# Kernel optimization log

Hardware: AMD Instinct MI355X
Metric: run time of the kernel (lower is better)

The kernel has to match this reference:

```python
import jax, jax.numpy as jnp
import numpy as np
from jax import lax

RES = 7
SCALE = 1.0 / 16.0


def _Fk(t):
    # antiderivative of the triangular bilinear kernel k(t)=max(0,1-|t|),
    # evaluated as integral from -1 to t (clamped to kernel support)
    t = jnp.clip(t, -1.0, 1.0)
    return jnp.where(t < 0, 0.5 * (t + 1.0) ** 2, 1.0 - 0.5 * (1.0 - t) ** 2)


def _bin_weights(lo, hi, L):
    # lo, hi: [R] roi start/end (feature coords). Returns ([R, RES, L], [R])
    bw = (hi - lo) / RES
    starts = lo[:, None] + bw[:, None] * jnp.arange(RES, dtype=lo.dtype)  # [R,RES]
    ends = starts + bw[:, None]
    idx = jnp.arange(L, dtype=lo.dtype)  # pixel centers
    # exact integral of bilinear kernel centered at each pixel over each bin
    W = _Fk(ends[:, :, None] - idx) - _Fk(starts[:, :, None] - idx)  # [R,RES,L]
    return W, bw


def prroi_pool(feat, bbox):
    # Precise RoI pooling: exact integral of bilinearly-interpolated feature
    # over each bin, which is separable in y and x.
    B, C, H, Wf = feat.shape
    R = bbox.shape[0]
    n = R // B  # boxes per frame (rois are grouped per frame, as in torch code)
    x1 = bbox[:, 0] * SCALE
    y1 = bbox[:, 1] * SCALE
    x2 = (bbox[:, 0] + bbox[:, 2]) * SCALE  # bbox stores (x1,y1,w,h)
    y2 = (bbox[:, 1] + bbox[:, 3]) * SCALE
    Wx, bwx = _bin_weights(x1, x2, Wf)
    Wy, bwy = _bin_weights(y1, y2, H)
    Wx = Wx.reshape(B, n, RES, Wf)
    Wy = Wy.reshape(B, n, RES, H)
    pooled = jnp.einsum('bnph,bchw,bnqw->bncpq', Wy, feat, Wx)  # [B,n,C,7,7]
    area = (bwx * bwy).reshape(B, n)[:, :, None, None, None]
    pooled = jnp.where(area > 0, pooled / jnp.maximum(area, 1e-12), 0.0)
    return pooled.reshape(R, C, RES, RES)


def _conv(x, w, pad):
    return lax.conv_general_dilated(x, w, (1, 1), ((pad, pad), (pad, pad)),
                                    dimension_numbers=('NCHW', 'OIHW', 'NCHW'))


def _cbn(x, w, s, b, pad):
    # conv (no bias) + FrozenBatchNorm (per-channel affine)
    return _conv(x, w, pad) * s[:, None, None] + b[:, None, None]


def _deconv2x2(x, w):
    # PyTorch ConvTranspose2d(k=2, s=2, p=0); w: [Cin, Cout, 2, 2]
    wc = jnp.flip(w, (2, 3)).transpose(1, 0, 2, 3)  # -> [Cout, Cin, 2, 2]
    return lax.conv_general_dilated(x, wc, (1, 1), ((1, 1), (1, 1)),
                                    lhs_dilation=(2, 2),
                                    dimension_numbers=('NCHW', 'OIHW', 'NCHW'))


def setup_inputs() -> dict:
    key = jax.random.key(0)
    ks = jax.random.split(key, 20)
    B, C, H, W = 16, 256, 36, 36
    R = 512  # 32 boxes per frame
    nb, bc = 3, 128
    g = 0.05
    feat = jax.random.normal(ks[0], (B, C, H, W), jnp.float32)
    u = jax.random.uniform(ks[1], (R, 4), jnp.float32)
    # (x1, y1, w, h) in image coords for a 576x576 search region
    bbox = jnp.concatenate([u[:, :2] * 400.0, 32.0 + u[:, 2:] * 128.0], axis=1)
    w1 = jax.random.normal(ks[2], (nb, bc, C, 1, 1), jnp.float32) * g
    s1 = jax.random.uniform(ks[3], (nb, bc), jnp.float32) * 0.5 + 0.5
    b1 = jax.random.normal(ks[4], (nb, bc), jnp.float32) * g
    w2 = jax.random.normal(ks[5], (nb, bc, bc, 3, 3), jnp.float32) * g
    s2 = jax.random.uniform(ks[6], (nb, bc), jnp.float32) * 0.5 + 0.5
    b2 = jax.random.normal(ks[7], (nb, bc), jnp.float32) * g
    w3 = jax.random.normal(ks[8], (nb, C, bc, 1, 1), jnp.float32) * g
    s3 = jax.random.uniform(ks[9], (nb, C), jnp.float32) * 0.5 + 0.5
    b3 = jax.random.normal(ks[10], (nb, C), jnp.float32) * g
    wt = jax.random.normal(ks[11], (C, 256, 2, 2), jnp.float32) * g
    bt = jax.random.normal(ks[12], (256,), jnp.float32) * g
    wm = jax.random.normal(ks[13], (1, 256, 1, 1), jnp.float32) * g
    bm = jax.random.normal(ks[14], (1,), jnp.float32) * g
    return dict(feat=feat, bbox=bbox, w1=w1, s1=s1, b1=b1, w2=w2, s2=s2, b2=b2,
                w3=w3, s3=s3, b3=b3, wt=wt, bt=bt, wm=wm, bm=bm)


def reference(feat, bbox, w1, s1, b1, w2, s2, b2, w3, s3, b3, wt, bt, wm, bm):
    x = prroi_pool(feat, bbox)  # [R, 256, 7, 7]
    # 3 bottleneck blocks with frozen BN (stride 1, no downsample: in==out)
    for i in range(w1.shape[0]):
        out = jax.nn.relu(_cbn(x, w1[i], s1[i], b1[i], 0))
        out = jax.nn.relu(_cbn(out, w2[i], s2[i], b2[i], 1))
        out = _cbn(out, w3[i], s3[i], b3[i], 0)
        x = jax.nn.relu(out + x)
    x = jax.nn.relu(_deconv2x2(x, wt) + bt[:, None, None])  # [R, 256, 14, 14]
    logits = _conv(x, wm, 0) + bm[:, None, None]  # [R, 1, 14, 14]
    return jax.nn.sigmoid(logits)  # eval-mode output
```

## Files before the change

### kernel.cpp

```cpp
#include <hip/hip_runtime.h>
#include <math.h>

#define RESQ 7
#define CH   256
#define NROI 512
#define BC   128
#define NB   3
#define NT   512

typedef __bf16 bh8  __attribute__((ext_vector_type(8)));
typedef float  f16v __attribute__((ext_vector_type(16)));

#define BAR() do { \
    asm volatile("s_waitcnt lgkmcnt(0)" ::: "memory"); \
    __builtin_amdgcn_s_barrier(); \
    asm volatile("" ::: "memory"); \
} while (0)

#define A1OFF 0
#define A2OFF 196608
#define A3OFF 1081344
#define ATOFF 1277952
#define WS_BYTES 1802240
#define FTOFF 1802240
#define WS_FULL 12419072
#define PRE_ELEMS 901120

#define XS_OFF 0
#define T1_OFF 25088
#define T2_OFF 45824
#define WY_OFF 58368
#define WX_OFF 59376
#define LG_OFF 60384
#define LDS_BYTES 64480

#define SWZ(row) (((row) & 15) << 4)

__device__ __forceinline__ float Fk(float t) {
    t = fminf(1.f, fmaxf(-1.f, t));
    float a = t + 1.f, b = 1.f - t;
    return (t < 0.f) ? 0.5f * a * a : 1.f - 0.5f * b * b;
}
__device__ __forceinline__ unsigned short bf16bits(float a) {
    return __builtin_bit_cast(unsigned short, (__bf16)a);
}
__device__ __forceinline__ unsigned int pk2(float a, float b) {
    return (unsigned int)bf16bits(a) | ((unsigned int)bf16bits(b) << 16);
}
__device__ __forceinline__ float b2f(unsigned int s) {
    return __builtin_bit_cast(float, s << 16);
}
__device__ __forceinline__ bh8 ld_bh8(const unsigned char* p) { return *(const bh8*)p; }
__device__ __forceinline__ bh8 cvt8(const float* p) {
    float4 a = *(const float4*)p;
    float4 b = *(const float4*)(p + 4);
    bh8 r;
    r[0]=(__bf16)a.x; r[1]=(__bf16)a.y; r[2]=(__bf16)a.z; r[3]=(__bf16)a.w;
    r[4]=(__bf16)b.x; r[5]=(__bf16)b.y; r[6]=(__bf16)b.z; r[7]=(__bf16)b.w;
    return r;
}
__device__ __forceinline__ bh8 gather8(const float* p, int stride) {
    bh8 r;
    #pragma unroll
    for (int j = 0; j < 8; ++j) r[j] = (__bf16)p[j * stride];
    return r;
}

__device__ __forceinline__ void epi_store(const f16v acc, int chbase, int h,
        const float* sarr, const float* barr, unsigned char* rowbase, int rswz) {
    #pragma unroll
    for (int g = 0; g < 4; ++g) {
        const int ch = chbase + 8*g + 4*h;
        const float4 sv = *(const float4*)(sarr + ch);
        const float4 bv = *(const float4*)(barr + ch);
        float v0 = fmaxf(fmaf(acc[4*g+0], sv.x, bv.x), 0.f);
        float v1 = fmaxf(fmaf(acc[4*g+1], sv.y, bv.y), 0.f);
        float v2 = fmaxf(fmaf(acc[4*g+2], sv.z, bv.z), 0.f);
        float v3 = fmaxf(fmaf(acc[4*g+3], sv.w, bv.w), 0.f);
        *(uint2*)(rowbase + ((2*ch) ^ rswz)) = make_uint2(pk2(v0,v1), pk2(v2,v3));
    }
}
__device__ __forceinline__ void epi_res(const f16v acc, int chbase, int h,
        const float* sarr, const float* barr, unsigned char* rowbase, int rswz) {
    #pragma unroll
    for (int g = 0; g < 4; ++g) {
        const int ch = chbase + 8*g + 4*h;
        const float4 sv = *(const float4*)(sarr + ch);
        const float4 bv = *(const float4*)(barr + ch);
        unsigned char* p = rowbase + ((2*ch) ^ rswz);
        const uint2 old = *(const uint2*)p;
        float v0 = fmaxf(fmaf(acc[4*g+0], sv.x, bv.x) + b2f(old.x & 0xFFFFu), 0.f);
        float v1 = fmaxf(fmaf(acc[4*g+1], sv.y, bv.y) + b2f(old.x >> 16), 0.f);
        float v2 = fmaxf(fmaf(acc[4*g+2], sv.z, bv.z) + b2f(old.y & 0xFFFFu), 0.f);
        float v3 = fmaxf(fmaf(acc[4*g+3], sv.w, bv.w) + b2f(old.y >> 16), 0.f);
        *(uint2*)p = make_uint2(pk2(v0,v1), pk2(v2,v3));
    }
}
__device__ __forceinline__ float dq_part(const f16v acc, int chbase, int h,
        const float* bt, const float* wm) {
    float part = 0.f;
    #pragma unroll
    for (int g = 0; g < 4; ++g) {
        const int ch = chbase + 8*g + 4*h;
        const float4 btv = *(const float4*)(bt + ch);
        const float4 wmv = *(const float4*)(wm + ch);
        part = fmaf(wmv.x, fmaxf(acc[4*g+0] + btv.x, 0.f), part);
        part = fmaf(wmv.y, fmaxf(acc[4*g+1] + btv.y, 0.f), part);
        part = fmaf(wmv.z, fmaxf(acc[4*g+2] + btv.z, 0.f), part);
        part = fmaf(wmv.w, fmaxf(acc[4*g+3] + btv.w, 0.f), part);
    }
    return part;
}

extern "C" __global__ void prep_all(const float* __restrict__ feat,
                                    const float* __restrict__ w1,
                                    const float* __restrict__ w2,
                                    const float* __restrict__ w3,
                                    const float* __restrict__ wt,
                                    unsigned char* __restrict__ ws,
                                    int do_ft) {
    __shared__ unsigned short tile[36 * 256];
    if (do_ft && blockIdx.x < 576) {
        const int b = blockIdx.x / 36, y = blockIdx.x % 36;
        const int c = threadIdx.x;
        const float* src = feat + (size_t)(b * 256 + c) * 1296 + y * 36;
        float4 fv[9];
        #pragma unroll
        for (int i = 0; i < 9; ++i) fv[i] = *(const float4*)(src + i * 4);
        #pragma unroll
        for (int i = 0; i < 9; ++i) {
            tile[(i*4+0)*256 + c] = bf16bits(fv[i].x);
            tile[(i*4+1)*256 + c] = bf16bits(fv[i].y);
            tile[(i*4+2)*256 + c] = bf16bits(fv[i].z);
            tile[(i*4+3)*256 + c] = bf16bits(fv[i].w);
        }
        __syncthreads();
        unsigned short* dst = (unsigned short*)(ws + FTOFF) + (size_t)(b*36 + y)*36*256;
        for (int x = 0; x < 36; ++x) dst[x*256 + c] = tile[x*256 + c];
        return;
    }
    const int base = do_ft ? 576 : 0;
    const int nb = gridDim.x - base;
    __bf16* wb = (__bf16*)ws;
    for (int i = (blockIdx.x - base) * blockDim.x + threadIdx.x; i < PRE_ELEMS;
         i += nb * blockDim.x) {
        float v; int dst;
        if (i < 98304) {
            int e = i;
            int j = e & 7, lane = (e>>3)&63, t = (e>>9)&15, mt = (e>>13)&3, ib = e>>15;
            int m = mt*32 + (lane&31), k = t*16 + 8*(lane>>5) + j;
            v = w1[(ib*BC + m)*CH + k];
            dst = (A1OFF>>1) + e;
        } else if (i < 98304 + 442368) {
            int e = i - 98304;
            int j = e & 7, lane = (e>>3)&63, t = (e>>9)&7, mt = (e>>12)&3;
            int rem = e >> 14;
            int ib = rem / 9, tap = rem - ib*9;
            int m = mt*32 + (lane&31), ci = t*16 + 8*(lane>>5) + j;
            v = w2[((ib*BC + m)*BC + ci)*9 + tap];
            dst = (A2OFF>>1) + e;
        } else if (i < 98304 + 442368 + 98304) {
            int e = i - (98304 + 442368);
            int j = e & 7, lane = (e>>3)&63, t = (e>>9)&7, mt = (e>>12)&7, ib = e>>15;
            int m = mt*32 + (lane&31), ci = t*16 + 8*(lane>>5) + j;
            v = w3[(ib*CH + m)*BC + ci];
            dst = (A3OFF>>1) + e;
        } else {
            int e = i - (98304 + 442368 + 98304);
            int j = e & 7, lane = (e>>3)&63, t = (e>>9)&15, mt = (e>>13)&7, quad = e>>16;
            int co = mt*32 + (lane&31), ci = t*16 + 8*(lane>>5) + j;
            v = wt[ci*1024 + co*4 + quad];
            dst = (ATOFF>>1) + e;
        }
        wb[dst] = (__bf16)v;
    }
}

template<int USE_WS, int USE_FT>
__global__ __launch_bounds__(NT, 2)
void masknet_mfma(const float* __restrict__ feat,
                  const float* __restrict__ bbox,
                  const float* __restrict__ w1, const float* __restrict__ s1, const float* __restrict__ b1,
                  const float* __restrict__ w2, const float* __restrict__ s2, const float* __restrict__ b2,
                  const float* __restrict__ w3, const float* __restrict__ s3, const float* __restrict__ b3,
                  const float* __restrict__ wt, const float* __restrict__ bt,
                  const float* __restrict__ wm, const float* __restrict__ bm,
                  const unsigned char* __restrict__ ws,
                  float* __restrict__ out)
{
    __shared__ __align__(16) unsigned char smem[LDS_BYTES];
    float* wyb = (float*)(smem + WY_OFF);
    float* wxb = (float*)(smem + WX_OFF);
    float* lgf = (float*)(smem + LG_OFF);

    const int tid  = threadIdx.x;
    const int r    = blockIdx.x;
    const int bfr  = r >> 5;
    const int lane = tid & 63;
    const int ln   = lane & 31;
    const int h    = lane >> 5;
    const int w_   = tid >> 6;
    const int cb   = 16 * h;

    const float S = 1.f / 16.f;
    const float bx = bbox[r*4+0], by = bbox[r*4+1];
    const float bw_ = bbox[r*4+2], bh_ = bbox[r*4+3];
    const float x1 = bx * S, y1 = by * S;
    const float bwx = (bw_ * S) * (1.f / RESQ);
    const float bwy = (bh_ * S) * (1.f / RESQ);
    const float area = bwx * bwy;
    const float inv_area = (area > 0.f) ? 1.f / fmaxf(area, 1e-12f) : 0.f;

    if (tid < 252) {
        int p = tid / 36, i = tid - p * 36;
        float st = y1 + bwy * p, en = st + bwy;
        wyb[tid] = Fk(en - (float)i) - Fk(st - (float)i);
    } else if (tid >= 256 && tid < 508) {
        int t = tid - 256;
        int q = t / 36, i = t - q * 36;
        float st = x1 + bwx * q, en = st + bwx;
        wxb[t] = Fk(en - (float)i) - Fk(st - (float)i);
    }
    {
        uint4* z = (uint4*)(smem + T1_OFF);
        for (int o = tid; o < 1296; o += NT) z[o] = make_uint4(0,0,0,0);
        for (int o = tid; o < 1024; o += NT) lgf[o] = 0.f;
    }
    BAR();

    if (USE_FT) {
        const unsigned short* ft = (const unsigned short*)(ws + FTOFF) + (size_t)bfr * (1296 * 256);
        const int g = w_ * 2 + h;
        #pragma unroll 1
        for (int k = 0; k < 4; ++k) {
            const int s = g + 16 * k;
            if (s >= 49) break;
            const int p = s / 7, q = s - p * 7;
            const float sy = y1 + bwy * p, sx = x1 + bwx * q;
            const int ylo = max(0, (int)floorf(sy)), yhi = min(35, (int)ceilf(sy + bwy));
            const int xlo = max(0, (int)floorf(sx)), xhi = min(35, (int)ceilf(sx + bwx));
            float wyv[4], wxv[4];
            #pragma unroll
            for (int j = 0; j < 4; ++j) {
                const int y = ylo + j, x = xlo + j;
                wyv[j] = (y <= yhi) ? wyb[p*36 + y] * inv_area : 0.f;
                wxv[j] = (x <= xhi) ? wxb[q*36 + x] : 0.f;
            }
            float ac0=0.f,ac1=0.f,ac2=0.f,ac3=0.f,ac4=0.f,ac5=0.f,ac6=0.f,ac7=0.f;
            #pragma unroll
            for (int yy = 0; yy < 4; ++yy) {
                const int y = min(ylo + yy, 35);
                const unsigned short* rowp = ft + (size_t)(y * 36) * 256 + ln * 8;
                #pragma unroll
                for (int xx = 0; xx < 4; ++xx) {
                    const int x = min(xlo + xx, 35);
                    const float wgt = wyv[yy] * wxv[xx];
                    const uint4 v = *(const uint4*)(rowp + x * 256);
                    ac0 = fmaf(wgt, b2f(v.x & 0xFFFFu), ac0);
                    ac1 = fmaf(wgt, b2f(v.x >> 16),     ac1);
                    ac2 = fmaf(wgt, b2f(v.y & 0xFFFFu), ac2);
                    ac3 = fmaf(wgt, b2f(v.y >> 16),     ac3);
                    ac4 = fmaf(wgt, b2f(v.z & 0xFFFFu), ac4);
                    ac5 = fmaf(wgt, b2f(v.z >> 16),     ac5);
                    ac6 = fmaf(wgt, b2f(v.w & 0xFFFFu), ac6);
                    ac7 = fmaf(wgt, b2f(v.w >> 16),     ac7);
                }
            }
            *(uint4*)(smem + XS_OFF + s * 512 + ((16 * ln) ^ SWZ(s))) =
                make_uint4(pk2(ac0,ac1), pk2(ac2,ac3), pk2(ac4,ac5), pk2(ac6,ac7));
        }
    } else {
        const float* fb = feat + (size_t)bfr * CH * 36 * 36;
        for (int o = tid; o < CH * 49; o += NT) {
            int c = o / 49, s = o - c * 49;
            int p = s / 7, q = s - p * 7;
            float sy = y1 + bwy * p, sx = x1 + bwx * q;
            int ylo = max(0, (int)floorf(sy)), yhi = min(35, (int)ceilf(sy + bwy));
            int xlo = max(0, (int)floorf(sx)), xhi = min(35, (int)ceilf(sx + bwx));
            const float* fc = fb + c * 1296;
            float acc = 0.f;
            for (int y = ylo; y <= yhi; ++y) {
                float wyv = wyb[p * 36 + y];
                for (int x = xlo; x <= xhi; ++x)
                    acc = fmaf(wyv * wxb[q * 36 + x], fc[y * 36 + x], acc);
            }
            *(unsigned short*)(smem + XS_OFF + s * 512 + ((2 * c) ^ SWZ(s))) =
                bf16bits(acc * inv_area);
        }
    }

    const int mt12 = w_ & 3, nt12 = w_ >> 2;
    const int col12 = nt12 * 32 + ln;
    const int ncl12 = min(col12, 48);
    const int mg = w_ >> 1, ng = w_ & 1;
    const int col3 = ng * 32 + ln;
    const int ncl3 = min(col3, 48);

    bh8 pf[4] = {};
    if (USE_WS) {
        #pragma unroll
        for (int t = 0; t < 4; ++t)
            pf[t] = ld_bh8(ws + A1OFF + ((((0*4 + mt12)*16 + t)*64 + lane) << 4));
    }
    BAR();

    #pragma unroll 1
    for (int ib = 0; ib < NB; ++ib) {
        {
            const unsigned char* bb = smem + XS_OFF + ncl12 * 512;
            const int bswz = SWZ(ncl12);
            f16v acc = {};
            #pragma unroll
            for (int t = 0; t < 16; ++t) {
                bh8 a;
                if (USE_WS) a = (t < 4) ? pf[t]
                                        : ld_bh8(ws + A1OFF + ((((ib*4 + mt12)*16 + t)*64 + lane) << 4));
                else        a = cvt8(w1 + (size_t)(ib*BC + mt12*32 + ln)*CH + t*16 + 8*h);
                bh8 b = ld_bh8(bb + ((t*32 + cb) ^ bswz));
                acc = __builtin_amdgcn_mfma_f32_32x32x16_bf16(a, b, acc, 0, 0, 0);
            }
            if (col12 < 49) {
                const int row = (col12/7 + 1)*9 + (col12 - (col12/7)*7) + 1;
                epi_store(acc, mt12*32, h, s1 + ib*BC, b1 + ib*BC,
                          smem + T1_OFF + row*256, SWZ(row));
            }
        }
        if (USE_WS) {
            #pragma unroll
            for (int t = 0; t < 4; ++t)
                pf[t] = ld_bh8(ws + A2OFF + (((((ib*9+0)*4 + mt12)*8 + t)*64 + lane) << 4));
        }
        BAR();

        {
            const int tr0 = (ncl12/7)*9 + (ncl12 - (ncl12/7)*7);
            f16v acc = {};
            #pragma unroll 1
            for (int ty = 0; ty < 3; ++ty) {
                #pragma unroll
                for (int tx = 0; tx < 3; ++tx) {
                    const int tap = ty*3 + tx;
                    bh8 aw[8];
                    #pragma unroll
                    for (int t = 0; t < 8; ++t) {
                        if (USE_WS) aw[t] = (ty == 0 && tx == 0 && t < 4) ? pf[t]
                                          : ld_bh8(ws + A2OFF + (((((ib*9+tap)*4 + mt12)*8 + t)*64 + lane) << 4));
                        else        aw[t] = gather8(w2 + ((size_t)(ib*BC + mt12*32 + ln)*BC + t*16 + 8*h)*9 + tap, 9);
                    }
                    const int row = tr0 + ty*9 + tx;
                    const unsigned char* bb = smem + T1_OFF + row*256;
                    const int rs = SWZ(row);
                    #pragma unroll
                    for (int t = 0; t < 8; ++t) {
                        bh8 b = ld_bh8(bb + ((t*32 + cb) ^ rs));
                        acc = __builtin_amdgcn_mfma_f32_32x32x16_bf16(aw[t], b, acc, 0, 0, 0);
                    }
                }
            }
            if (col12 < 49) {
                epi_store(acc, mt12*32, h, s2 + ib*BC, b2 + ib*BC,
                          smem + T2_OFF + col12*256, SWZ(col12));
            }
        }
        if (USE_WS) {
            #pragma unroll
            for (int t = 0; t < 4; ++t)
                pf[t] = ld_bh8(ws + A3OFF + ((((ib*8 + 2*mg+0)*8 + t)*64 + lane) << 4));
        }
        BAR();

        {
            const unsigned char* bb = smem + T2_OFF + ncl3 * 256;
            const int bswz = SWZ(ncl3);
            f16v acc0 = {}, acc1 = {};
            #pragma unroll
            for (int t = 0; t < 8; ++t) {
                bh8 a0, a1;
                if (USE_WS) {
                    a0 = (t < 4) ? pf[t]
                                 : ld_bh8(ws + A3OFF + ((((ib*8 + 2*mg+0)*8 + t)*64 + lane) << 4));
                    a1 = ld_bh8(ws + A3OFF + ((((ib*8 + 2*mg+1)*8 + t)*64 + lane) << 4));
                } else {
                    a0 = cvt8(w3 + (size_t)(ib*CH + (2*mg+0)*32 + ln)*BC + t*16 + 8*h);
                    a1 = cvt8(w3 + (size_t)(ib*CH + (2*mg+1)*32 + ln)*BC + t*16 + 8*h);
                }
                bh8 b = ld_bh8(bb + ((t*32 + cb) ^ bswz));
                acc0 = __builtin_amdgcn_mfma_f32_32x32x16_bf16(a0, b, acc0, 0, 0, 0);
                acc1 = __builtin_amdgcn_mfma_f32_32x32x16_bf16(a1, b, acc1, 0, 0, 0);
            }
            if (col3 < 49) {
                unsigned char* rowb = smem + XS_OFF + col3*512;
                const int rs = SWZ(col3);
                epi_res(acc0, (2*mg+0)*32, h, s3 + ib*CH, b3 + ib*CH, rowb, rs);
                epi_res(acc1, (2*mg+1)*32, h, s3 + ib*CH, b3 + ib*CH, rowb, rs);
            }
        }
        if (USE_WS) {
            #pragma unroll
            for (int t = 0; t < 4; ++t) {
                if (ib < NB - 1)
                    pf[t] = ld_bh8(ws + A1OFF + (((((ib+1)*4 + mt12)*16 + t)*64 + lane) << 4));
                else
                    pf[t] = ld_bh8(ws + ATOFF + ((((0*8 + 2*mg+0)*16 + t)*64 + lane) << 4));
            }
        }
        BAR();
    }

    {
        const unsigned char* bb = smem + XS_OFF + ncl3 * 512;
        const int bswz = SWZ(ncl3);
        bh8 bf[16];
        #pragma unroll
        for (int t = 0; t < 16; ++t)
            bf[t] = ld_bh8(bb + ((t*32 + cb) ^ bswz));
        #pragma unroll 1
        for (int quad = 0; quad < 4; ++quad) {
            f16v acc0 = {}, acc1 = {};
            #pragma unroll
            for (int t = 0; t < 16; ++t) {
                bh8 a0, a1;
                if (USE_WS) {
                    a0 = (quad == 0 && t < 4) ? pf[t]
                                 : ld_bh8(ws + ATOFF + ((((quad*8 + 2*mg+0)*16 + t)*64 + lane) << 4));
                    a1 = ld_bh8(ws + ATOFF + ((((quad*8 + 2*mg+1)*16 + t)*64 + lane) << 4));
                } else {
                    a0 = gather8(wt + (size_t)(t*16 + 8*h)*1024 + ((2*mg+0)*32 + ln)*4 + quad, 1024);
                    a1 = gather8(wt + (size_t)(t*16 + 8*h)*1024 + ((2*mg+1)*32 + ln)*4 + quad, 1024);
                }
                acc0 = __builtin_amdgcn_mfma_f32_32x32x16_bf16(a0, bf[t], acc0, 0, 0, 0);
                acc1 = __builtin_amdgcn_mfma_f32_32x32x16_bf16(a1, bf[t], acc1, 0, 0, 0);
            }
            float p0 = dq_part(acc0, (2*mg+0)*32, h, bt, wm)
                     + dq_part(acc1, (2*mg+1)*32, h, bt, wm);
            p0 += __shfl_down(p0, 32);
            if (h == 0 && col3 < 49) lgf[(quad*4 + mg)*64 + col3] = p0;
        }
    }
    BAR();

    if (tid < 196) {
        const int quad = tid / 49, s = tid - quad*49;
        const float val = lgf[(quad*4+0)*64 + s] + lgf[(quad*4+1)*64 + s]
                        + lgf[(quad*4+2)*64 + s] + lgf[(quad*4+3)*64 + s] + bm[0];
        const int p = s / 7, q = s - p*7;
        const int dy = quad >> 1, dx = quad & 1;
        out[(size_t)r * 196 + (2*p + dy)*14 + (2*q + dx)] = 1.f / (1.f + expf(-val));
    }
}

extern "C" void kernel_launch(void* const* d_in, const int* in_sizes, int n_in,
                              void* d_out, int out_size, void* d_ws, size_t ws_size,
                              hipStream_t stream) {
    const float* feat = (const float*)d_in[0];
    const float* bbox = (const float*)d_in[1];
    const float* w1   = (const float*)d_in[2];
    const float* s1   = (const float*)d_in[3];
    const float* b1   = (const float*)d_in[4];
    const float* w2   = (const float*)d_in[5];
    const float* s2   = (const float*)d_in[6];
    const float* b2   = (const float*)d_in[7];
    const float* w3   = (const float*)d_in[8];
    const float* s3   = (const float*)d_in[9];
    const float* b3   = (const float*)d_in[10];
    const float* wt   = (const float*)d_in[11];
    const float* bt   = (const float*)d_in[12];
    const float* wm   = (const float*)d_in[13];
    const float* bm   = (const float*)d_in[14];
    float* out = (float*)d_out;

    if (ws_size >= (size_t)WS_FULL) {
        unsigned char* ws = (unsigned char*)d_ws;
        hipLaunchKernelGGL(prep_all, dim3(1024), dim3(256), 0, stream,
                           feat, w1, w2, w3, wt, ws, 1);
        hipLaunchKernelGGL((masknet_mfma<1,1>), dim3(NROI), dim3(NT), 0, stream,
                           feat, bbox, w1, s1, b1, w2, s2, b2, w3, s3, b3,
                           wt, bt, wm, bm, ws, out);
    } else if (ws_size >= (size_t)WS_BYTES) {
        unsigned char* ws = (unsigned char*)d_ws;
        hipLaunchKernelGGL(prep_all, dim3(448), dim3(256), 0, stream,
                           feat, w1, w2, w3, wt, ws, 0);
        hipLaunchKernelGGL((masknet_mfma<1,0>), dim3(NROI), dim3(NT), 0, stream,
                           feat, bbox, w1, s1, b1, w2, s2, b2, w3, s3, b3,
                           wt, bt, wm, bm, ws, out);
    } else {
        hipLaunchKernelGGL((masknet_mfma<0,0>), dim3(NROI), dim3(NT), 0, stream,
                           feat, bbox, w1, s1, b1, w2, s2, b2, w3, s3, b3,
                           wt, bt, wm, bm, (const unsigned char*)nullptr, out);
    }
}
```

Measured before the change: 128.3 us.

## Process two RoIs per block to reuse weight fragments across MFMAs

```diff
diff --git a/kernel.cpp b/kernel.cpp
--- a/kernel.cpp
+++ b/kernel.cpp
@@ -27,12 +27,15 @@
 #define PRE_ELEMS 901120
 
 #define XS_OFF 0
-#define T1_OFF 25088
-#define T2_OFF 45824
-#define WY_OFF 58368
-#define WX_OFF 59376
-#define LG_OFF 60384
-#define LDS_BYTES 64480
+#define XS_RR  25088
+#define T1_OFF 50176
+#define T1_RR  20736
+#define T2_OFF 91648
+#define T2_RR  12544
+#define WY_OFF 116736
+#define WX_OFF 118752
+#define LG_OFF 120768
+#define LDS_BYTES 128960
 
 #define SWZ(row) (((row) & 15) << 4)
 
@@ -189,103 +192,115 @@
                   float* __restrict__ out)
 {
     __shared__ __align__(16) unsigned char smem[LDS_BYTES];
-    float* wyb = (float*)(smem + WY_OFF);
-    float* wxb = (float*)(smem + WX_OFF);
-    float* lgf = (float*)(smem + LG_OFF);
 
     const int tid  = threadIdx.x;
-    const int r    = blockIdx.x;
-    const int bfr  = r >> 5;
+    const int r0   = blockIdx.x * 2;
+    const int bfr  = r0 >> 5;
     const int lane = tid & 63;
     const int ln   = lane & 31;
     const int h    = lane >> 5;
     const int w_   = tid >> 6;
     const int cb   = 16 * h;
-
-    const float S = 1.f / 16.f;
-    const float bx = bbox[r*4+0], by = bbox[r*4+1];
-    const float bw_ = bbox[r*4+2], bh_ = bbox[r*4+3];
-    const float x1 = bx * S, y1 = by * S;
-    const float bwx = (bw_ * S) * (1.f / RESQ);
-    const float bwy = (bh_ * S) * (1.f / RESQ);
-    const float area = bwx * bwy;
-    const float inv_area = (area > 0.f) ? 1.f / fmaxf(area, 1e-12f) : 0.f;
-
-    if (tid < 252) {
-        int p = tid / 36, i = tid - p * 36;
-        float st = y1 + bwy * p, en = st + bwy;
-        wyb[tid] = Fk(en - (float)i) - Fk(st - (float)i);
-    } else if (tid >= 256 && tid < 508) {
-        int t = tid - 256;
-        int q = t / 36, i = t - q * 36;
-        float st = x1 + bwx * q, en = st + bwx;
-        wxb[t] = Fk(en - (float)i) - Fk(st - (float)i);
+    const float S  = 1.f / 16.f;
+
+    #pragma unroll
+    for (int rr = 0; rr < 2; ++rr) {
+        const int r = r0 + rr;
+        const float y1 = bbox[r*4+1] * S;
+        const float x1 = bbox[r*4+0] * S;
+        const float bwy = (bbox[r*4+3] * S) * (1.f / RESQ);
+        const float bwx = (bbox[r*4+2] * S) * (1.f / RESQ);
+        float* wyb = (float*)(smem + WY_OFF + rr*1008);
+        float* wxb = (float*)(smem + WX_OFF + rr*1008);
+        if (tid < 252) {
+            int p = tid / 36, i = tid - p * 36;
+            float st = y1 + bwy * p, en = st + bwy;
+            wyb[tid] = Fk(en - (float)i) - Fk(st - (float)i);
+        } else if (tid >= 256 && tid < 508) {
+            int t = tid - 256;
+            int q = t / 36, i = t - q * 36;
+            float st = x1 + bwx * q, en = st + bwx;
+            wxb[t] = Fk(en - (float)i) - Fk(st - (float)i);
+        }
     }
     {
         uint4* z = (uint4*)(smem + T1_OFF);
-        for (int o = tid; o < 1296; o += NT) z[o] = make_uint4(0,0,0,0);
-        for (int o = tid; o < 1024; o += NT) lgf[o] = 0.f;
+        for (int o = tid; o < 2592; o += NT) z[o] = make_uint4(0,0,0,0);
+        float* lg = (float*)(smem + LG_OFF);
+        for (int o = tid; o < 2048; o += NT) lg[o] = 0.f;
     }
     BAR();
 
-    if (USE_FT) {
-        const unsigned short* ft = (const unsigned short*)(ws + FTOFF) + (size_t)bfr * (1296 * 256);
-        const int g = w_ * 2 + h;
-        #pragma unroll 1
-        for (int k = 0; k < 4; ++k) {
-            const int s = g + 16 * k;
-            if (s >= 49) break;
-            const int p = s / 7, q = s - p * 7;
-            const float sy = y1 + bwy * p, sx = x1 + bwx * q;
-            const int ylo = max(0, (int)floorf(sy)), yhi = min(35, (int)ceilf(sy + bwy));
-            const int xlo = max(0, (int)floorf(sx)), xhi = min(35, (int)ceilf(sx + bwx));
-            float wyv[4], wxv[4];
-            #pragma unroll
-            for (int j = 0; j < 4; ++j) {
-                const int y = ylo + j, x = xlo + j;
-                wyv[j] = (y <= yhi) ? wyb[p*36 + y] * inv_area : 0.f;
-                wxv[j] = (x <= xhi) ? wxb[q*36 + x] : 0.f;
-            }
-            float ac0=0.f,ac1=0.f,ac2=0.f,ac3=0.f,ac4=0.f,ac5=0.f,ac6=0.f,ac7=0.f;
-            #pragma unroll
-            for (int yy = 0; yy < 4; ++yy) {
-                const int y = min(ylo + yy, 35);
-                const unsigned short* rowp = ft + (size_t)(y * 36) * 256 + ln * 8;
+    #pragma unroll
+    for (int rr = 0; rr < 2; ++rr) {
+        const int r = r0 + rr;
+        const float y1 = bbox[r*4+1] * S;
+        const float x1 = bbox[r*4+0] * S;
+        const float bwy = (bbox[r*4+3] * S) * (1.f / RESQ);
+        const float bwx = (bbox[r*4+2] * S) * (1.f / RESQ);
+        const float area = bwx * bwy;
+        const float inv_area = (area > 0.f) ? 1.f / fmaxf(area, 1e-12f) : 0.f;
+        float* wyb = (float*)(smem + WY_OFF + rr*1008);
+        float* wxb = (float*)(smem + WX_OFF + rr*1008);
+        if (USE_FT) {
+            const unsigned short* ft = (const unsigned short*)(ws + FTOFF) + (size_t)bfr * (1296 * 256);
+            const int g = w_ * 2 + h;
+            #pragma unroll 1
+            for (int k = 0; k < 4; ++k) {
+                const int s = g + 16 * k;
+                if (s >= 49) break;
+                const int p = s / 7, q = s - p * 7;
+                const float sy = y1 + bwy * p, sx = x1 + bwx * q;
+                const int ylo = max(0, (int)floorf(sy)), yhi = min(35, (int)ceilf(sy + bwy));
+                const int xlo = max(0, (int)floorf(sx)), xhi = min(35, (int)ceilf(sx + bwx));
+                float wyv[4], wxv[4];
                 #pragma unroll
-                for (int xx = 0; xx < 4; ++xx) {
-                    const int x = min(xlo + xx, 35);
-                    const float wgt = wyv[yy] * wxv[xx];
-                    const uint4 v = *(const uint4*)(rowp + x * 256);
-                    ac0 = fmaf(wgt, b2f(v.x & 0xFFFFu), ac0);
-                    ac1 = fmaf(wgt, b2f(v.x >> 16),     ac1);
-                    ac2 = fmaf(wgt, b2f(v.y & 0xFFFFu), ac2);
-                    ac3 = fmaf(wgt, b2f(v.y >> 16),     ac3);
-                    ac4 = fmaf(wgt, b2f(v.z & 0xFFFFu), ac4);
-                    ac5 = fmaf(wgt, b2f(v.z >> 16),     ac5);
-                    ac6 = fmaf(wgt, b2f(v.w & 0xFFFFu), ac6);
-                    ac7 = fmaf(wgt, b2f(v.w >> 16),     ac7);
+                for (int j = 0; j < 4; ++j) {
+                    const int y = ylo + j, x = xlo + j;
+                    wyv[j] = (y <= yhi) ? wyb[p*36 + y] * inv_area : 0.f;
+                    wxv[j] = (x <= xhi) ? wxb[q*36 + x] : 0.f;
                 }
-            }
-            *(uint4*)(smem + XS_OFF + s * 512 + ((16 * ln) ^ SWZ(s))) =
-                make_uint4(pk2(ac0,ac1), pk2(ac2,ac3), pk2(ac4,ac5), pk2(ac6,ac7));
-        }
-    } else {
-        const float* fb = feat + (size_t)bfr * CH * 36 * 36;
-        for (int o = tid; o < CH * 49; o += NT) {
-            int c = o / 49, s = o - c * 49;
-            int p = s / 7, q = s - p * 7;
-            float sy = y1 + bwy * p, sx = x1 + bwx * q;
-            int ylo = max(0, (int)floorf(sy)), yhi = min(35, (int)ceilf(sy + bwy));
-            int xlo = max(0, (int)floorf(sx)), xhi = min(35, (int)ceilf(sx + bwx));
-            const float* fc = fb + c * 1296;
-            float acc = 0.f;
-            for (int y = ylo; y <= yhi; ++y) {
-                float wyv = wyb[p * 36 + y];
-                for (int x = xlo; x <= xhi; ++x)
-                    acc = fmaf(wyv * wxb[q * 36 + x], fc[y * 36 + x], acc);
-            }
-            *(unsigned short*)(smem + XS_OFF + s * 512 + ((2 * c) ^ SWZ(s))) =
-                bf16bits(acc * inv_area);
+                float ac0=0.f,ac1=0.f,ac2=0.f,ac3=0.f,ac4=0.f,ac5=0.f,ac6=0.f,ac7=0.f;
+                #pragma unroll
+                for (int yy = 0; yy < 4; ++yy) {
+                    const int y = min(ylo + yy, 35);
+                    const unsigned short* rowp = ft + (size_t)(y * 36) * 256 + ln * 8;
+                    #pragma unroll
+                    for (int xx = 0; xx < 4; ++xx) {
+                        const int x = min(xlo + xx, 35);
+                        const float wgt = wyv[yy] * wxv[xx];
+                        const uint4 v = *(const uint4*)(rowp + x * 256);
+                        ac0 = fmaf(wgt, b2f(v.x & 0xFFFFu), ac0);
+                        ac1 = fmaf(wgt, b2f(v.x >> 16),     ac1);
+                        ac2 = fmaf(wgt, b2f(v.y & 0xFFFFu), ac2);
+                        ac3 = fmaf(wgt, b2f(v.y >> 16),     ac3);
+                        ac4 = fmaf(wgt, b2f(v.z & 0xFFFFu), ac4);
+                        ac5 = fmaf(wgt, b2f(v.z >> 16),     ac5);
+                        ac6 = fmaf(wgt, b2f(v.w & 0xFFFFu), ac6);
+                        ac7 = fmaf(wgt, b2f(v.w >> 16),     ac7);
+                    }
+                }
+                *(uint4*)(smem + XS_OFF + rr*XS_RR + s * 512 + ((16 * ln) ^ SWZ(s))) =
+                    make_uint4(pk2(ac0,ac1), pk2(ac2,ac3), pk2(ac4,ac5), pk2(ac6,ac7));
+            }
+        } else {
+            const float* fb = feat + (size_t)bfr * CH * 36 * 36;
+            for (int o = tid; o < CH * 49; o += NT) {
+                int c = o / 49, s = o - c * 49;
+                int p = s / 7, q = s - p * 7;
+                float sy = y1 + bwy * p, sx = x1 + bwx * q;
+                int ylo = max(0, (int)floorf(sy)), yhi = min(35, (int)ceilf(sy + bwy));
+                int xlo = max(0, (int)floorf(sx)), xhi = min(35, (int)ceilf(sx + bwx));
+                const float* fc = fb + c * 1296;
+                float acc = 0.f;
+                for (int y = ylo; y <= yhi; ++y) {
+                    float wyv = wyb[p * 36 + y];
+                    for (int x = xlo; x <= xhi; ++x)
+                        acc = fmaf(wyv * wxb[q * 36 + x], fc[y * 36 + x], acc);
+                }
+                *(unsigned short*)(smem + XS_OFF + rr*XS_RR + s * 512 + ((2 * c) ^ SWZ(s))) =
+                    bf16bits(acc * inv_area);
+            }
         }
     }
 
@@ -307,22 +322,27 @@
     #pragma unroll 1
     for (int ib = 0; ib < NB; ++ib) {
         {
-            const unsigned char* bb = smem + XS_OFF + ncl12 * 512;
+            const unsigned char* bb0 = smem + XS_OFF + 0*XS_RR + ncl12 * 512;
+            const unsigned char* bb1 = smem + XS_OFF + 1*XS_RR + ncl12 * 512;
             const int bswz = SWZ(ncl12);
-            f16v acc = {};
+            f16v acc0 = {}, acc1 = {};
             #pragma unroll
             for (int t = 0; t < 16; ++t) {
                 bh8 a;
                 if (USE_WS) a = (t < 4) ? pf[t]
                                         : ld_bh8(ws + A1OFF + ((((ib*4 + mt12)*16 + t)*64 + lane) << 4));
                 else        a = cvt8(w1 + (size_t)(ib*BC + mt12*32 + ln)*CH + t*16 + 8*h);
-                bh8 b = ld_bh8(bb + ((t*32 + cb) ^ bswz));
-                acc = __builtin_amdgcn_mfma_f32_32x32x16_bf16(a, b, acc, 0, 0, 0);
+                bh8 b0 = ld_bh8(bb0 + ((t*32 + cb) ^ bswz));
+                bh8 b1 = ld_bh8(bb1 + ((t*32 + cb) ^ bswz));
+                acc0 = __builtin_amdgcn_mfma_f32_32x32x16_bf16(a, b0, acc0, 0, 0, 0);
+                acc1 = __builtin_amdgcn_mfma_f32_32x32x16_bf16(a, b1, acc1, 0, 0, 0);
             }
             if (col12 < 49) {
                 const int row = (col12/7 + 1)*9 + (col12 - (col12/7)*7) + 1;
-                epi_store(acc, mt12*32, h, s1 + ib*BC, b1 + ib*BC,
-                          smem + T1_OFF + row*256, SWZ(row));
+                epi_store(acc0, mt12*32, h, s1 + ib*BC, b1 + ib*BC,
+                          smem + T1_OFF + 0*T1_RR + row*256, SWZ(row));
+                epi_store(acc1, mt12*32, h, s1 + ib*BC, b1 + ib*BC,
+                          smem + T1_OFF + 1*T1_RR + row*256, SWZ(row));
             }
         }
         if (USE_WS) {
@@ -334,7 +354,7 @@
 
         {
             const int tr0 = (ncl12/7)*9 + (ncl12 - (ncl12/7)*7);
-            f16v acc = {};
+            f16v acc0 = {}, acc1 = {};
             #pragma unroll 1
             for (int ty = 0; ty < 3; ++ty) {
                 #pragma unroll
@@ -348,18 +368,23 @@
                         else        aw[t] = gather8(w2 + ((size_t)(ib*BC + mt12*32 + ln)*BC + t*16 + 8*h)*9 + tap, 9);
                     }
                     const int row = tr0 + ty*9 + tx;
-                    const unsigned char* bb = smem + T1_OFF + row*256;
+                    const unsigned char* bb0 = smem + T1_OFF + 0*T1_RR + row*256;
+                    const unsigned char* bb1 = smem + T1_OFF + 1*T1_RR + row*256;
                     const int rs = SWZ(row);
                     #pragma unroll
                     for (int t = 0; t < 8; ++t) {
-                        bh8 b = ld_bh8(bb + ((t*32 + cb) ^ rs));
-                        acc = __builtin_amdgcn_mfma_f32_32x32x16_bf16(aw[t], b, acc, 0, 0, 0);
+                        bh8 b0 = ld_bh8(bb0 + ((t*32 + cb) ^ rs));
+                        bh8 b1 = ld_bh8(bb1 + ((t*32 + cb) ^ rs));
+                        acc0 = __builtin_amdgcn_mfma_f32_32x32x16_bf16(aw[t], b0, acc0, 0, 0, 0);
+                        acc1 = __builtin_amdgcn_mfma_f32_32x32x16_bf16(aw[t], b1, acc1, 0, 0, 0);
                     }
                 }
             }
             if (col12 < 49) {
-                epi_store(acc, mt12*32, h, s2 + ib*BC, b2 + ib*BC,
-                          smem + T2_OFF + col12*256, SWZ(col12));
+                epi_store(acc0, mt12*32, h, s2 + ib*BC, b2 + ib*BC,
+                          smem + T2_OFF + 0*T2_RR + col12*256, SWZ(col12));
+                epi_store(acc1, mt12*32, h, s2 + ib*BC, b2 + ib*BC,
+                          smem + T2_OFF + 1*T2_RR + col12*256, SWZ(col12));
             }
         }
         if (USE_WS) {
@@ -370,9 +395,10 @@
         BAR();
 
         {
-            const unsigned char* bb = smem + T2_OFF + ncl3 * 256;
+            const unsigned char* bb0 = smem + T2_OFF + 0*T2_RR + ncl3 * 256;
+            const unsigned char* bb1 = smem + T2_OFF + 1*T2_RR + ncl3 * 256;
             const int bswz = SWZ(ncl3);
-            f16v acc0 = {}, acc1 = {};
+            f16v acc00 = {}, acc01 = {}, acc10 = {}, acc11 = {};
             #pragma unroll
             for (int t = 0; t < 8; ++t) {
                 bh8 a0, a1;
@@ -384,15 +410,21 @@
                     a0 = cvt8(w3 + (size_t)(ib*CH + (2*mg+0)*32 + ln)*BC + t*16 + 8*h);
                     a1 = cvt8(w3 + (size_t)(ib*CH + (2*mg+1)*32 + ln)*BC + t*16 + 8*h);
                 }
-                bh8 b = ld_bh8(bb + ((t*32 + cb) ^ bswz));
-                acc0 = __builtin_amdgcn_mfma_f32_32x32x16_bf16(a0, b, acc0, 0, 0, 0);
-                acc1 = __builtin_amdgcn_mfma_f32_32x32x16_bf16(a1, b, acc1, 0, 0, 0);
+                bh8 b0 = ld_bh8(bb0 + ((t*32 + cb) ^ bswz));
+                bh8 b1 = ld_bh8(bb1 + ((t*32 + cb) ^ bswz));
+                acc00 = __builtin_amdgcn_mfma_f32_32x32x16_bf16(a0, b0, acc00, 0, 0, 0);
+                acc01 = __builtin_amdgcn_mfma_f32_32x32x16_bf16(a0, b1, acc01, 0, 0, 0);
+                acc10 = __builtin_amdgcn_mfma_f32_32x32x16_bf16(a1, b0, acc10, 0, 0, 0);
+                acc11 = __builtin_amdgcn_mfma_f32_32x32x16_bf16(a1, b1, acc11, 0, 0, 0);
             }
             if (col3 < 49) {
-                unsigned char* rowb = smem + XS_OFF + col3*512;
                 const int rs = SWZ(col3);
-                epi_res(acc0, (2*mg+0)*32, h, s3 + ib*CH, b3 + ib*CH, rowb, rs);
-                epi_res(acc1, (2*mg+1)*32, h, s3 + ib*CH, b3 + ib*CH, rowb, rs);
+                unsigned char* rb0 = smem + XS_OFF + 0*XS_RR + col3*512;
+                unsigned char* rb1 = smem + XS_OFF + 1*XS_RR + col3*512;
+                epi_res(acc00, (2*mg+0)*32, h, s3 + ib*CH, b3 + ib*CH, rb0, rs);
+                epi_res(acc10, (2*mg+1)*32, h, s3 + ib*CH, b3 + ib*CH, rb0, rs);
+                epi_res(acc01, (2*mg+0)*32, h, s3 + ib*CH, b3 + ib*CH, rb1, rs);
+                epi_res(acc11, (2*mg+1)*32, h, s3 + ib*CH, b3 + ib*CH, rb1, rs);
             }
         }
         if (USE_WS) {
@@ -408,15 +440,12 @@
     }
 
     {
-        const unsigned char* bb = smem + XS_OFF + ncl3 * 512;
+        const unsigned char* bb0 = smem + XS_OFF + 0*XS_RR + ncl3 * 512;
+        const unsigned char* bb1 = smem + XS_OFF + 1*XS_RR + ncl3 * 512;
         const int bswz = SWZ(ncl3);
-        bh8 bf[16];
-        #pragma unroll
-        for (int t = 0; t < 16; ++t)
-            bf[t] = ld_bh8(bb + ((t*32 + cb) ^ bswz));
         #pragma unroll 1
         for (int quad = 0; quad < 4; ++quad) {
-            f16v acc0 = {}, acc1 = {};
+            f16v acc00 = {}, acc01 = {}, acc10 = {}, acc11 = {};
             #pragma unroll
             for (int t = 0; t < 16; ++t) {
                 bh8 a0, a1;
@@ -428,24 +457,39 @@
                     a0 = gather8(wt + (size_t)(t*16 + 8*h)*1024 + ((2*mg+0)*32 + ln)*4 + quad, 1024);
                     a1 = gather8(wt + (size_t)(t*16 + 8*h)*1024 + ((2*mg+1)*32 + ln)*4 + quad, 1024);
                 }
-                acc0 = __builtin_amdgcn_mfma_f32_32x32x16_bf16(a0, bf[t], acc0, 0, 0, 0);
-                acc1 = __builtin_amdgcn_mfma_f32_32x32x16_bf16(a1, bf[t], acc1, 0, 0, 0);
-            }
-            float p0 = dq_part(acc0, (2*mg+0)*32, h, bt, wm)
-                     + dq_part(acc1, (2*mg+1)*32, h, bt, wm);
+                bh8 b0 = ld_bh8(bb0 + ((t*32 + cb) ^ bswz));
+                bh8 b1 = ld_bh8(bb1 + ((t*32 + cb) ^ bswz));
+                acc00 = __builtin_amdgcn_mfma_f32_32x32x16_bf16(a0, b0, acc00, 0, 0, 0);
+                acc01 = __builtin_amdgcn_mfma_f32_32x32x16_bf16(a0, b1, acc01, 0, 0, 0);
+                acc10 = __builtin_amdgcn_mfma_f32_32x32x16_bf16(a1, b0, acc10, 0, 0, 0);
+                acc11 = __builtin_amdgcn_mfma_f32_32x32x16_bf16(a1, b1, acc11, 0, 0, 0);
+            }
+            float p0 = dq_part(acc00, (2*mg+0)*32, h, bt, wm)
+                     + dq_part(acc10, (2*mg+1)*32, h, bt, wm);
+            float p1 = dq_part(acc01, (2*mg+0)*32, h, bt, wm)
+                     + dq_part(acc11, (2*mg+1)*32, h, bt, wm);
             p0 += __shfl_down(p0, 32);
-            if (h == 0 && col3 < 49) lgf[(quad*4 + mg)*64 + col3] = p0;
+            p1 += __shfl_down(p1, 32);
+            if (h == 0 && col3 < 49) {
+                ((float*)(smem + LG_OFF + 0*4096))[(quad*4 + mg)*64 + col3] = p0;
+                ((float*)(smem + LG_OFF + 1*4096))[(quad*4 + mg)*64 + col3] = p1;
+            }
         }
     }
     BAR();
 
-    if (tid < 196) {
-        const int quad = tid / 49, s = tid - quad*49;
-        const float val = lgf[(quad*4+0)*64 + s] + lgf[(quad*4+1)*64 + s]
-                        + lgf[(quad*4+2)*64 + s] + lgf[(quad*4+3)*64 + s] + bm[0];
-        const int p = s / 7, q = s - p*7;
-        const int dy = quad >> 1, dx = quad & 1;
-        out[(size_t)r * 196 + (2*p + dy)*14 + (2*q + dx)] = 1.f / (1.f + expf(-val));
+    #pragma unroll
+    for (int rr = 0; rr < 2; ++rr) {
+        if (tid < 196) {
+            const float* lg = (const float*)(smem + LG_OFF + rr*4096);
+            const int quad = tid / 49, s = tid - quad*49;
+            const float val = lg[(quad*4+0)*64 + s] + lg[(quad*4+1)*64 + s]
+                            + lg[(quad*4+2)*64 + s] + lg[(quad*4+3)*64 + s] + bm[0];
+            const int p = s / 7, q = s - p*7;
+            const int dy = quad >> 1, dx = quad & 1;
+            out[(size_t)(r0 + rr) * 196 + (2*p + dy)*14 + (2*q + dx)] =
+                1.f / (1.f + expf(-val));
+        }
     }
 }
 
@@ -473,18 +517,18 @@
         unsigned char* ws = (unsigned char*)d_ws;
         hipLaunchKernelGGL(prep_all, dim3(1024), dim3(256), 0, stream,
                            feat, w1, w2, w3, wt, ws, 1);
-        hipLaunchKernelGGL((masknet_mfma<1,1>), dim3(NROI), dim3(NT), 0, stream,
+        hipLaunchKernelGGL((masknet_mfma<1,1>), dim3(NROI/2), dim3(NT), 0, stream,
                            feat, bbox, w1, s1, b1, w2, s2, b2, w3, s3, b3,
                            wt, bt, wm, bm, ws, out);
     } else if (ws_size >= (size_t)WS_BYTES) {
         unsigned char* ws = (unsigned char*)d_ws;
         hipLaunchKernelGGL(prep_all, dim3(448), dim3(256), 0, stream,
                            feat, w1, w2, w3, wt, ws, 0);
-        hipLaunchKernelGGL((masknet_mfma<1,0>), dim3(NROI), dim3(NT), 0, stream,
+        hipLaunchKernelGGL((masknet_mfma<1,0>), dim3(NROI/2), dim3(NT), 0, stream,
                            feat, bbox, w1, s1, b1, w2, s2, b2, w3, s3, b3,
                            wt, bt, wm, bm, ws, out);
     } else {
-        hipLaunchKernelGGL((masknet_mfma<0,0>), dim3(NROI), dim3(NT), 0, stream,
+        hipLaunchKernelGGL((masknet_mfma<0,0>), dim3(NROI/2), dim3(NT), 0, stream,
                            feat, bbox, w1, s1, b1, w2, s2, b2, w3, s3, b3,
                            wt, bt, wm, bm, (const unsigned char*)nullptr, out);
     }
```

Measured after the change: 115.1 us. 10.3% less time.
